# Kernel tuning notes

Measured on AMD Instinct MI355X. Metric: run time of the kernel, lower is better.

The kernel has to match this reference:

```python
import jax, jax.numpy as jnp
import numpy as np

B, CIN, COUT, S, K, G = 2, 64, 64, 128, 3, 4  # batch, in_ch, out_ch, shapes(H=W), kernel, groups


def _conv1x1(w, x, b=None):
    # nn.Conv2d(kernel_size=1): w [O,C], x [B,C,H,W]
    y = jnp.einsum('oc,bchw->bohw', w, x)
    return y if b is None else y + b[None, :, None, None]


def _forward(fs, ft, w_q, w_k, w_v, rel_h, rel_w, weights1_real, weights1_imag,
             w0_w, w0_b, convv_w, convv_b, convv1_w, convv1_b, rate1, rate2):
    Bq, C, H, W = fs.shape
    q = _conv1x1(w_q, fs)  # [B,C,H,W]
    # key/value convs are 1x1 with no bias, so conv(pad(x)) == pad(conv(x))
    kf = jnp.pad(_conv1x1(w_k, fs), ((0, 0), (0, 0), (1, 1), (1, 1)))
    vf = jnp.pad(_conv1x1(w_v, fs), ((0, 0), (0, 0), (1, 1), (1, 1)))

    def unfold(xp):  # [B,C,H+2,W+2] -> [B,C,H,W,K,K] (torch .unfold(2,K,1).unfold(3,K,1))
        p = jnp.stack([xp[:, :, i:i + H, j:j + W] for i in range(K) for j in range(K)], axis=-1)
        return p.reshape(Bq, C, H, W, K, K)

    k = unfold(kf)
    v = unfold(vf)
    # relative position bias on the two channel halves (broadcast as in torch)
    k = jnp.concatenate([k[:, :C // 2] + rel_h, k[:, C // 2:] + rel_w], axis=1)
    k = k.reshape(Bq, G, C // G, H, W, K * K)
    v = v.reshape(Bq, G, C // G, H, W, K * K)
    qg = q.reshape(Bq, G, C // G, H, W, 1)
    attn = jax.nn.softmax(qg * k, axis=-1)                         # [B,G,C/G,H,W,9]
    out = jnp.einsum('bnchwk,bnchwk->bnchw', attn, v).reshape(Bq, C, H, W)

    # ---- spectral branch ----
    # Original code: einsum 'bchw,ohwi->bochw' (i is summed over weights only),
    # flatten to [B, o*c*H, W], fftshift over dims(1,2), reshape to [B,64,8192,128,2],
    # zero an EMPTY slice (rw=int(0.1*1)=0), ifftshift over dims(3,2,1), then
    # ifft2 with s=(H,W) which CROPS the 8192 dim to its first H rows.
    # The roll arithmetic composes to: net-zero shift on o and w axes, and a
    # +C/2 shift on the c axis; the crop then selects c = C//2, h = 0..H-1.
    # => out1 = Re ifft2( fft2(out)[:, C//2] * sum_i W[o,:,h,w] ).
    fs_ft = jnp.fft.fft2(out, norm='ortho')                        # [B,C,H,W] complex
    wsum = (weights1_real + 1j * weights1_imag).sum(axis=1)        # [CIN,H,W] (sum over 'i')
    out_ft = fs_ft[:, C // 2][:, None, :, :] * wsum[None]          # [B,CIN,H,W]
    out1 = jnp.fft.ifft2(out_ft, norm='ortho').real                # [B,CIN,H,W]

    out_cv = _conv1x1(convv_w, out, convv_b)                       # con_vv
    out2 = _conv1x1(w0_w, out_cv, w0_b)                            # w0
    out2 = _conv1x1(convv1_w, out2, convv1_b)                      # con_vv1

    make_fs = rate1[0] * out1 + rate2[0] * out2                    # [B,CIN,H,W]
    make_fs = jnp.transpose(make_fs, (0, 2, 3, 1))                 # [B,H,W,C]
    ftv = ft.reshape(Bq, H, W, C)                                  # out_channels != 320 branch
    return jnp.mean((make_fs - ftv) ** 2)


def setup_inputs() -> dict:
    key = jax.random.key(0)
    ks = jax.random.split(key, 12)
    n = lambda i, shape, s=1.0: jax.random.normal(ks[i], shape, dtype=jnp.float32) * s
    scale = 1.0 / (CIN * COUT)
    return {
        'fs': n(0, (B, CIN, S, S)),
        'ft': n(1, (B, S, S, COUT)),
        'w_q': n(2, (COUT, CIN), 0.1),
        'w_k': n(3, (COUT, CIN), 0.1),
        'w_v': n(4, (COUT, CIN), 0.1),
        'rel_h': n(5, (COUT // 2, 1, 1, K, 1)),
        'rel_w': n(6, (COUT // 2, 1, 1, 1, K)),
        'weights1_real': jax.random.uniform(ks[7], (CIN, COUT, S, S), dtype=jnp.float32) * scale,
        'weights1_imag': jax.random.uniform(ks[8], (CIN, COUT, S, S), dtype=jnp.float32) * scale,
        'w0_w': n(9, (COUT, CIN), 0.1),
        'w0_b': jnp.zeros((COUT,), jnp.float32),
        'convv_w': n(10, (CIN, COUT), 0.1),
        'convv_b': jnp.zeros((CIN,), jnp.float32),
        'convv1_w': n(11, (CIN, COUT), 0.1),
        'convv1_b': jnp.zeros((CIN,), jnp.float32),
        'rate1': jnp.full((1,), 0.5, jnp.float32),
        'rate2': jnp.full((1,), 0.5, jnp.float32),
    }


def reference(fs, ft, w_q, w_k, w_v, rel_h, rel_w, weights1_real, weights1_imag,
              w0_w, w0_b, convv_w, convv_b, convv1_w, convv1_b, rate1, rate2):
    return _forward(fs, ft, w_q, w_k, w_v, rel_h, rel_w, weights1_real, weights1_imag,
                    w0_w, w0_b, convv_w, convv_b, convv1_w, convv1_b, rate1, rate2)
```

## Files before the change

### kernel.cpp

```cpp
#include <hip/hip_runtime.h>
#include <math.h>

constexpr int HW   = 128 * 128;
constexpr int NCHW = 2 * 64 * HW;

constexpr size_t OFF_Q    = 0;
constexpr size_t OFF_K    = 2097152;
constexpr size_t OFF_V    = 4194304;
constexpr size_t OFF_FTT  = 4194304;
constexpr size_t OFF_OUT  = 6291456;
constexpr size_t OFF_OUT2 = 8388608;
constexpr size_t OFF_R    = 8388608;
constexpr size_t OFF_F    = 10485760;
constexpr size_t OFF_M    = 10551296;
constexpr size_t OFF_BC   = 10555392;
constexpr size_t OFF_Z    = 0;

__global__ __launch_bounds__(256) void k_gemm64(
    const float* __restrict__ x, const float* __restrict__ w,
    const float* __restrict__ bias, float* __restrict__ y)
{
    __shared__ float xs[64][64];
    __shared__ float wl[64][65];
    int blk = blockIdx.x;
    int b = blk >> 8;
    int px0 = (blk & 255) << 6;
    int t = threadIdx.x;
    for (int i = t; i < 4096; i += 256) {
        int r = i >> 6, cix = i & 63;
        wl[r][cix] = w[i];
        xs[r][cix] = x[b * (64 * HW) + r * HW + px0 + cix];
    }
    __syncthreads();
    int pxq = t & 15, rq = t >> 4;
    float acc[4][4];
    #pragma unroll
    for (int i = 0; i < 4; i++)
        for (int j = 0; j < 4; j++) acc[i][j] = 0.f;
    for (int ci = 0; ci < 64; ci++) {
        float4 xv = *reinterpret_cast<const float4*>(&xs[ci][pxq * 4]);
        #pragma unroll
        for (int i = 0; i < 4; i++) {
            float wv = wl[rq * 4 + i][ci];
            acc[i][0] += wv * xv.x; acc[i][1] += wv * xv.y;
            acc[i][2] += wv * xv.z; acc[i][3] += wv * xv.w;
        }
    }
    #pragma unroll
    for (int i = 0; i < 4; i++) {
        int co = rq * 4 + i;
        float bb = bias ? bias[co] : 0.f;
        float* p = y + b * (64 * HW) + co * HW + px0 + pxq * 4;
        p[0] = acc[i][0] + bb; p[1] = acc[i][1] + bb;
        p[2] = acc[i][2] + bb; p[3] = acc[i][3] + bb;
    }
}

__global__ __launch_bounds__(256) void k_attn(
    const float* __restrict__ q, const float* __restrict__ kc, const float* __restrict__ vc,
    const float* __restrict__ rel_h, const float* __restrict__ rel_w,
    float* __restrict__ out)
{
    int idx = blockIdx.x * 256 + threadIdx.x;
    if (idx >= NCHW) return;
    int w = idx & 127;
    int h = (idx >> 7) & 127;
    int c = (idx >> 14) & 63;
    float qv = q[idx];
    float s[9], vv[9];
    #pragma unroll
    for (int ki = 0; ki < 3; ki++) {
        #pragma unroll
        for (int kj = 0; kj < 3; kj++) {
            int hh = h + ki - 1, ww = w + kj - 1;
            bool inb = (hh >= 0 && hh < 128 && ww >= 0 && ww < 128);
            int nidx = (idx & ~(HW - 1)) + hh * 128 + ww;
            float kvv = inb ? kc[nidx] : 0.f;
            float vvv = inb ? vc[nidx] : 0.f;
            float rel = (c < 32) ? rel_h[c * 3 + ki] : rel_w[(c - 32) * 3 + kj];
            s[ki * 3 + kj] = qv * (kvv + rel);
            vv[ki * 3 + kj] = vvv;
        }
    }
    float m = s[0];
    #pragma unroll
    for (int i = 1; i < 9; i++) m = fmaxf(m, s[i]);
    float den = 0.f, num = 0.f;
    #pragma unroll
    for (int i = 0; i < 9; i++) { float e = __expf(s[i] - m); den += e; num += e * vv[i]; }
    out[idx] = num / den;
}

__global__ __launch_bounds__(256) void k_tft(const float* __restrict__ ft, float* __restrict__ ftT)
{
    __shared__ float tile[64][65];
    int blk = blockIdx.x; int b = blk >> 8; int p0 = (blk & 255) << 6;
    int t = threadIdx.x;
    for (int e = t; e < 4096; e += 256) {
        int pp = e >> 6, cc = e & 63;
        tile[pp][cc] = ft[(b * HW + p0 + pp) * 64 + cc];
    }
    __syncthreads();
    for (int e = t; e < 4096; e += 256) {
        int cc = e >> 6, pp = e & 63;
        ftT[b * (64 * HW) + cc * HW + p0 + pp] = tile[pp][cc];
    }
}

__global__ __launch_bounds__(128) void k_fftrow_fwd(const float* __restrict__ out, float* __restrict__ R)
{
    int bh = blockIdx.x; int b = bh >> 7, h = bh & 127;
    int k = threadIdx.x;
    __shared__ float xr[128];
    xr[k] = out[((b * 64 + 32) << 14) + h * 128 + k];
    __syncthreads();
    float s0, c0; __sincosf(-6.2831853071795864769f * (float)k / 128.0f, &s0, &c0);
    float twr = 1.f, twi = 0.f, ar = 0.f, ai = 0.f;
    for (int n = 0; n < 128; n++) {
        float xv = xr[n];
        ar += xv * twr; ai += xv * twi;
        float nr = twr * c0 - twi * s0;
        twi = twr * s0 + twi * c0; twr = nr;
    }
    float2* Rp = (float2*)R;
    Rp[(b << 14) + h * 128 + k] = make_float2(ar, ai);
}

__global__ __launch_bounds__(128) void k_fftcol_fwd(const float* __restrict__ R, float* __restrict__ F)
{
    int bk = blockIdx.x; int b = bk >> 7, k2 = bk & 127;
    int k1 = threadIdx.x;
    __shared__ float2 col[128];
    const float2* Rp = (const float2*)R;
    col[k1] = Rp[(b << 14) + k1 * 128 + k2];
    __syncthreads();
    float s0, c0; __sincosf(-6.2831853071795864769f * (float)k1 / 128.0f, &s0, &c0);
    float twr = 1.f, twi = 0.f, ar = 0.f, ai = 0.f;
    for (int n = 0; n < 128; n++) {
        float2 xv = col[n];
        ar += xv.x * twr - xv.y * twi;
        ai += xv.x * twi + xv.y * twr;
        float nr = twr * c0 - twi * s0;
        twi = twr * s0 + twi * c0; twr = nr;
    }
    float2* Fp = (float2*)F;
    Fp[(b << 14) + k1 * 128 + k2] = make_float2(ar * (1.f / 128.f), ai * (1.f / 128.f));
}

__global__ __launch_bounds__(256) void k_combine(
    const float* __restrict__ convv_w, const float* __restrict__ convv_b,
    const float* __restrict__ w0_w, const float* __restrict__ w0_b,
    const float* __restrict__ convv1_w, const float* __restrict__ convv1_b,
    float* __restrict__ M, float* __restrict__ bc)
{
    __shared__ float T[64][65];
    __shared__ float t2[64];
    int t = threadIdx.x;
    for (int e = t; e < 4096; e += 256) {
        int i = e >> 6, j = e & 63;
        float a = 0.f;
        for (int kk = 0; kk < 64; kk++) a += w0_w[i * 64 + kk] * convv_w[kk * 64 + j];
        T[i][j] = a;
    }
    if (t < 64) {
        float a = 0.f;
        for (int kk = 0; kk < 64; kk++) a += w0_w[t * 64 + kk] * convv_b[kk];
        t2[t] = a + w0_b[t];
    }
    __syncthreads();
    for (int e = t; e < 4096; e += 256) {
        int i = e >> 6, j = e & 63;
        float a = 0.f;
        for (int kk = 0; kk < 64; kk++) a += convv1_w[i * 64 + kk] * T[kk][j];
        M[e] = a;
    }
    if (t < 64) {
        float a = 0.f;
        for (int kk = 0; kk < 64; kk++) a += convv1_w[t * 64 + kk] * t2[kk];
        bc[t] = a + convv1_b[t];
    }
}

__global__ __launch_bounds__(128) void k_wsum_ifftrow(
    const float* __restrict__ w1r, const float* __restrict__ w1i,
    const float* __restrict__ F, float* __restrict__ Z)
{
    int blk = blockIdx.x; int c = blk >> 7, h = blk & 127;
    int t = threadIdx.x;
    float sr = 0.f, si = 0.f;
    int base = (c << 20) + h * 128 + t;
    #pragma unroll 8
    for (int o = 0; o < 64; o++) {
        sr += w1r[base + (o << 14)];
        si += w1i[base + (o << 14)];
    }
    __shared__ float4 g[128];
    const float2* Fp = (const float2*)F;
    float2 f0 = Fp[h * 128 + t];
    float2 f1 = Fp[(1 << 14) + h * 128 + t];
    g[t] = make_float4(f0.x * sr - f0.y * si, f0.x * si + f0.y * sr,
                       f1.x * sr - f1.y * si, f1.x * si + f1.y * sr);
    __syncthreads();
    float s0, c0; __sincosf(6.2831853071795864769f * (float)t / 128.0f, &s0, &c0);
    float twr = 1.f, twi = 0.f;
    float a0r = 0.f, a0i = 0.f, a1r = 0.f, a1i = 0.f;
    for (int n = 0; n < 128; n++) {
        float4 gv = g[n];
        a0r += gv.x * twr - gv.y * twi;
        a0i += gv.x * twi + gv.y * twr;
        a1r += gv.z * twr - gv.w * twi;
        a1i += gv.z * twi + gv.w * twr;
        float nr = twr * c0 - twi * s0;
        twi = twr * s0 + twi * c0; twr = nr;
    }
    float2* Zp = (float2*)Z;
    Zp[(c << 14) + h * 128 + t]               = make_float2(a0r, a0i);
    Zp[((64 + c) << 14) + h * 128 + t]        = make_float2(a1r, a1i);
}

__global__ __launch_bounds__(256) void k_ifftcol_mse(
    const float* __restrict__ Zb, const float* __restrict__ out2,
    const float* __restrict__ ftT, const float* __restrict__ rate1,
    const float* __restrict__ rate2, float* __restrict__ result)
{
    int blk = blockIdx.x;
    int xc = blk & 3;
    int c  = (blk >> 2) & 63;
    int b  = blk >> 8;
    int t = threadIdx.x;
    int xl = t & 31;
    int yq = t >> 5;
    __shared__ float2 zs[128][33];
    const float2* Zp = (const float2*)Zb;
    int zbase = ((b * 64 + c) << 14) + xc * 32;
    for (int e = t; e < 4096; e += 256) {
        int hh = e >> 5, xx = e & 31;
        zs[hh][xx] = Zp[zbase + hh * 128 + xx];
    }
    __syncthreads();

    float twx[4], twy[4], stx[4], sty[4];
    float Sr[4][4], Si[4][4];
    #pragma unroll
    for (int j = 0; j < 4; j++) {
        int y0 = yq + 8 * j;
        float ss, cc;
        __sincosf(6.2831853071795864769f * (float)y0 / 128.0f, &ss, &cc);
        stx[j] = cc; sty[j] = ss;
        twx[j] = 1.f; twy[j] = 0.f;
        #pragma unroll
        for (int m = 0; m < 4; m++) { Sr[j][m] = 0.f; Si[j][m] = 0.f; }
    }
    for (int h = 0; h < 128; h += 4) {
        #pragma unroll
        for (int m = 0; m < 4; m++) {
            float2 z = zs[h + m][xl];
            #pragma unroll
            for (int j = 0; j < 4; j++) {
                Sr[j][m] += z.x * twx[j] - z.y * twy[j];
                Si[j][m] += z.x * twy[j] + z.y * twx[j];
                float nr = twx[j] * stx[j] - twy[j] * sty[j];
                twy[j]   = twx[j] * sty[j] + twy[j] * stx[j];
                twx[j]   = nr;
            }
        }
    }
    float r1 = rate1[0], r2 = rate2[0];
    int x = xc * 32 + xl;
    int obase = ((b * 64 + c) << 14) + x;
    float part = 0.f;
    #pragma unroll
    for (int j = 0; j < 4; j++) {
        int y0 = yq + 8 * j;
        float o[4];
        o[0] = Sr[j][0] + Sr[j][1] + Sr[j][2] + Sr[j][3];
        o[1] = Sr[j][0] - Si[j][1] - Sr[j][2] + Si[j][3];
        o[2] = Sr[j][0] - Sr[j][1] + Sr[j][2] - Sr[j][3];
        o[3] = Sr[j][0] + Si[j][1] - Sr[j][2] - Si[j][3];
        #pragma unroll
        for (int m = 0; m < 4; m++) {
            int y = y0 + 32 * m;
            float out1 = o[m] * (1.f / 128.f);
            int gi = obase + y * 128;
            float mk = r1 * out1 + r2 * out2[gi];
            float d = mk - ftT[gi];
            part += d * d;
        }
    }
    __shared__ float red[256];
    red[t] = part;
    __syncthreads();
    for (int s = 128; s > 0; s >>= 1) {
        if (t < s) red[t] += red[t + s];
        __syncthreads();
    }
    if (t == 0) atomicAdd(result, red[0] * (1.f / 2097152.f));
}

extern "C" void kernel_launch(void* const* d_in, const int* in_sizes, int n_in,
                              void* d_out, int out_size, void* d_ws, size_t ws_size,
                              hipStream_t stream) {
    const float* fs       = (const float*)d_in[0];
    const float* ft       = (const float*)d_in[1];
    const float* w_q      = (const float*)d_in[2];
    const float* w_k      = (const float*)d_in[3];
    const float* w_v      = (const float*)d_in[4];
    const float* rel_h    = (const float*)d_in[5];
    const float* rel_w    = (const float*)d_in[6];
    const float* w1r      = (const float*)d_in[7];
    const float* w1i      = (const float*)d_in[8];
    const float* w0_w     = (const float*)d_in[9];
    const float* w0_b     = (const float*)d_in[10];
    const float* convv_w  = (const float*)d_in[11];
    const float* convv_b  = (const float*)d_in[12];
    const float* convv1_w = (const float*)d_in[13];
    const float* convv1_b = (const float*)d_in[14];
    const float* rate1    = (const float*)d_in[15];
    const float* rate2    = (const float*)d_in[16];

    float* ws = (float*)d_ws;
    float* q    = ws + OFF_Q;
    float* kk   = ws + OFF_K;
    float* vv   = ws + OFF_V;
    float* ftT  = ws + OFF_FTT;
    float* out  = ws + OFF_OUT;
    float* out2 = ws + OFF_OUT2;
    float* R    = ws + OFF_R;
    float* F    = ws + OFF_F;
    float* M    = ws + OFF_M;
    float* bc   = ws + OFF_BC;
    float* Z    = ws + OFF_Z;

    k_gemm64<<<512, 256, 0, stream>>>(fs, w_q, nullptr, q);
    k_gemm64<<<512, 256, 0, stream>>>(fs, w_k, nullptr, kk);
    k_gemm64<<<512, 256, 0, stream>>>(fs, w_v, nullptr, vv);
    k_attn<<<8192, 256, 0, stream>>>(q, kk, vv, rel_h, rel_w, out);
    k_tft<<<512, 256, 0, stream>>>(ft, ftT);
    k_fftrow_fwd<<<256, 128, 0, stream>>>(out, R);
    k_fftcol_fwd<<<256, 128, 0, stream>>>(R, F);
    k_combine<<<1, 256, 0, stream>>>(convv_w, convv_b, w0_w, w0_b, convv1_w, convv1_b, M, bc);
    k_gemm64<<<512, 256, 0, stream>>>(out, M, bc, out2);
    k_wsum_ifftrow<<<8192, 128, 0, stream>>>(w1r, w1i, F, Z);
    hipMemsetAsync(d_out, 0, sizeof(float), stream);
    k_ifftcol_mse<<<512, 256, 0, stream>>>(Z, out2, ftT, rate1, rate2, (float*)d_out);
}
```

Baseline: 717.1 us.

## Fuse QKV projections, drop ft transpose, vectorize weight-sum reduction, stage combine weights

Merges the three separate 1x1 projection GEMMs into one kernel that loads the input tile once and writes q, k and v together. It also removes the ft transpose kernel and reads ft directly with a channel-strided index in the final MSE kernel. The dominant weight-sum kernel now reads w1r/w1i with float4 loads spread over four output groups and reduces them in shared memory. The tiny combine kernel now stages its weight matrices in shared memory. The strided ft reads may be less coalesced, and the weight-sum kernel uses more shared memory and an extra barrier.

```diff
diff --git a/kernel.cpp b/kernel.cpp
--- a/kernel.cpp
+++ b/kernel.cpp
@@ -7,7 +7,6 @@
 constexpr size_t OFF_Q    = 0;
 constexpr size_t OFF_K    = 2097152;
 constexpr size_t OFF_V    = 4194304;
-constexpr size_t OFF_FTT  = 4194304;
 constexpr size_t OFF_OUT  = 6291456;
 constexpr size_t OFF_OUT2 = 8388608;
 constexpr size_t OFF_R    = 8388608;
@@ -15,6 +14,52 @@
 constexpr size_t OFF_M    = 10551296;
 constexpr size_t OFF_BC   = 10555392;
 constexpr size_t OFF_Z    = 0;
+
+__global__ __launch_bounds__(256) void k_qkv(
+    const float* __restrict__ fs,
+    const float* __restrict__ w_q, const float* __restrict__ w_k, const float* __restrict__ w_v,
+    float* __restrict__ q, float* __restrict__ kk, float* __restrict__ vv)
+{
+    __shared__ float xs[64][64];
+    __shared__ float wl[3][64][65];
+    int blk = blockIdx.x;
+    int b = blk >> 8;
+    int px0 = (blk & 255) << 6;
+    int t = threadIdx.x;
+    for (int i = t; i < 4096; i += 256) {
+        int r = i >> 6, cix = i & 63;
+        wl[0][r][cix] = w_q[i];
+        wl[1][r][cix] = w_k[i];
+        wl[2][r][cix] = w_v[i];
+        xs[r][cix] = fs[b * (64 * HW) + r * HW + px0 + cix];
+    }
+    __syncthreads();
+    int pxq = t & 15, rq = t >> 4;
+    float aq[4][4], ak[4][4], av[4][4];
+    #pragma unroll
+    for (int i = 0; i < 4; i++)
+        for (int j = 0; j < 4; j++) { aq[i][j] = 0.f; ak[i][j] = 0.f; av[i][j] = 0.f; }
+    for (int ci = 0; ci < 64; ci++) {
+        float4 xv = *reinterpret_cast<const float4*>(&xs[ci][pxq * 4]);
+        #pragma unroll
+        for (int i = 0; i < 4; i++) {
+            float wq_ = wl[0][rq * 4 + i][ci];
+            float wk_ = wl[1][rq * 4 + i][ci];
+            float wv_ = wl[2][rq * 4 + i][ci];
+            aq[i][0] += wq_ * xv.x; aq[i][1] += wq_ * xv.y; aq[i][2] += wq_ * xv.z; aq[i][3] += wq_ * xv.w;
+            ak[i][0] += wk_ * xv.x; ak[i][1] += wk_ * xv.y; ak[i][2] += wk_ * xv.z; ak[i][3] += wk_ * xv.w;
+            av[i][0] += wv_ * xv.x; av[i][1] += wv_ * xv.y; av[i][2] += wv_ * xv.z; av[i][3] += wv_ * xv.w;
+        }
+    }
+    #pragma unroll
+    for (int i = 0; i < 4; i++) {
+        int co = rq * 4 + i;
+        size_t base = (size_t)b * (64 * HW) + (size_t)co * HW + px0 + pxq * 4;
+        *reinterpret_cast<float4*>(q  + base) = make_float4(aq[i][0], aq[i][1], aq[i][2], aq[i][3]);
+        *reinterpret_cast<float4*>(kk + base) = make_float4(ak[i][0], ak[i][1], ak[i][2], ak[i][3]);
+        *reinterpret_cast<float4*>(vv + base) = make_float4(av[i][0], av[i][1], av[i][2], av[i][3]);
+    }
+}
 
 __global__ __launch_bounds__(256) void k_gemm64(
     const float* __restrict__ x, const float* __restrict__ w,
@@ -91,22 +136,6 @@
     out[idx] = num / den;
 }
 
-__global__ __launch_bounds__(256) void k_tft(const float* __restrict__ ft, float* __restrict__ ftT)
-{
-    __shared__ float tile[64][65];
-    int blk = blockIdx.x; int b = blk >> 8; int p0 = (blk & 255) << 6;
-    int t = threadIdx.x;
-    for (int e = t; e < 4096; e += 256) {
-        int pp = e >> 6, cc = e & 63;
-        tile[pp][cc] = ft[(b * HW + p0 + pp) * 64 + cc];
-    }
-    __syncthreads();
-    for (int e = t; e < 4096; e += 256) {
-        int cc = e >> 6, pp = e & 63;
-        ftT[b * (64 * HW) + cc * HW + p0 + pp] = tile[pp][cc];
-    }
-}
-
 __global__ __launch_bounds__(128) void k_fftrow_fwd(const float* __restrict__ out, float* __restrict__ R)
 {
     int bh = blockIdx.x; int b = bh >> 7, h = bh & 127;
@@ -153,30 +182,40 @@
     const float* __restrict__ convv1_w, const float* __restrict__ convv1_b,
     float* __restrict__ M, float* __restrict__ bc)
 {
+    __shared__ float A[64][64];
+    __shared__ float Bm[64][64];
+    __shared__ float Cm[64][64];
     __shared__ float T[64][65];
     __shared__ float t2[64];
     int t = threadIdx.x;
     for (int e = t; e < 4096; e += 256) {
         int i = e >> 6, j = e & 63;
-        float a = 0.f;
-        for (int kk = 0; kk < 64; kk++) a += w0_w[i * 64 + kk] * convv_w[kk * 64 + j];
-        T[i][j] = a;
-    }
-    if (t < 64) {
-        float a = 0.f;
-        for (int kk = 0; kk < 64; kk++) a += w0_w[t * 64 + kk] * convv_b[kk];
-        t2[t] = a + w0_b[t];
+        A[i][j]  = convv_w[e];
+        Bm[i][j] = w0_w[e];
+        Cm[i][j] = convv1_w[e];
     }
     __syncthreads();
     for (int e = t; e < 4096; e += 256) {
         int i = e >> 6, j = e & 63;
         float a = 0.f;
-        for (int kk = 0; kk < 64; kk++) a += convv1_w[i * 64 + kk] * T[kk][j];
-        M[e] = a;
+        for (int kk = 0; kk < 64; kk++) a += Bm[i][kk] * A[kk][j];
+        T[i][j] = a;
     }
     if (t < 64) {
         float a = 0.f;
-        for (int kk = 0; kk < 64; kk++) a += convv1_w[t * 64 + kk] * t2[kk];
+        for (int kk = 0; kk < 64; kk++) a += Bm[t][kk] * convv_b[kk];
+        t2[t] = a + w0_b[t];
+    }
+    __syncthreads();
+    for (int e = t; e < 4096; e += 256) {
+        int i = e >> 6, j = e & 63;
+        float a = 0.f;
+        for (int kk = 0; kk < 64; kk++) a += Cm[i][kk] * T[kk][j];
+        M[e] = a;
+    }
+    if (t < 64) {
+        float a = 0.f;
+        for (int kk = 0; kk < 64; kk++) a += Cm[t][kk] * t2[kk];
         bc[t] = a + convv1_b[t];
     }
 }
@@ -187,40 +226,70 @@
 {
     int blk = blockIdx.x; int c = blk >> 7, h = blk & 127;
     int t = threadIdx.x;
-    float sr = 0.f, si = 0.f;
-    int base = (c << 20) + h * 128 + t;
+    int wq = t & 31, og = t >> 5;
+    const float4* r4 = (const float4*)(w1r + ((size_t)c << 20) + (h << 7));
+    const float4* i4 = (const float4*)(w1i + ((size_t)c << 20) + (h << 7));
+    float4 sr = make_float4(0.f, 0.f, 0.f, 0.f);
+    float4 si = make_float4(0.f, 0.f, 0.f, 0.f);
+    int base = ((og * 16) << 12) + wq;
     #pragma unroll 8
-    for (int o = 0; o < 64; o++) {
-        sr += w1r[base + (o << 14)];
-        si += w1i[base + (o << 14)];
-    }
-    __shared__ float4 g[128];
-    const float2* Fp = (const float2*)F;
-    float2 f0 = Fp[h * 128 + t];
-    float2 f1 = Fp[(1 << 14) + h * 128 + t];
-    g[t] = make_float4(f0.x * sr - f0.y * si, f0.x * si + f0.y * sr,
-                       f1.x * sr - f1.y * si, f1.x * si + f1.y * sr);
+    for (int oo = 0; oo < 16; oo++) {
+        float4 a = r4[base + (oo << 12)];
+        float4 bb = i4[base + (oo << 12)];
+        sr.x += a.x;  sr.y += a.y;  sr.z += a.z;  sr.w += a.w;
+        si.x += bb.x; si.y += bb.y; si.z += bb.z; si.w += bb.w;
+    }
+    __shared__ float4 redr[4][32];
+    __shared__ float4 redi[4][32];
+    __shared__ float2 g0[128];
+    __shared__ float2 g1[128];
+    redr[og][wq] = sr; redi[og][wq] = si;
+    __syncthreads();
+    if (t < 32) {
+        float4 r0 = redr[0][t], r1_ = redr[1][t], r2_ = redr[2][t], r3 = redr[3][t];
+        float4 i0 = redi[0][t], i1 = redi[1][t], i2 = redi[2][t], i3 = redi[3][t];
+        float sumr[4], sumi[4];
+        sumr[0] = r0.x + r1_.x + r2_.x + r3.x;
+        sumr[1] = r0.y + r1_.y + r2_.y + r3.y;
+        sumr[2] = r0.z + r1_.z + r2_.z + r3.z;
+        sumr[3] = r0.w + r1_.w + r2_.w + r3.w;
+        sumi[0] = i0.x + i1.x + i2.x + i3.x;
+        sumi[1] = i0.y + i1.y + i2.y + i3.y;
+        sumi[2] = i0.z + i1.z + i2.z + i3.z;
+        sumi[3] = i0.w + i1.w + i2.w + i3.w;
+        const float2* Fp = (const float2*)F;
+        #pragma unroll
+        for (int j = 0; j < 4; j++) {
+            int w = t * 4 + j;
+            float wr = sumr[j], wi = sumi[j];
+            float2 f0 = Fp[(h << 7) + w];
+            float2 f1 = Fp[(1 << 14) + (h << 7) + w];
+            g0[w] = make_float2(f0.x * wr - f0.y * wi, f0.x * wi + f0.y * wr);
+            g1[w] = make_float2(f1.x * wr - f1.y * wi, f1.x * wi + f1.y * wr);
+        }
+    }
     __syncthreads();
     float s0, c0; __sincosf(6.2831853071795864769f * (float)t / 128.0f, &s0, &c0);
     float twr = 1.f, twi = 0.f;
     float a0r = 0.f, a0i = 0.f, a1r = 0.f, a1i = 0.f;
     for (int n = 0; n < 128; n++) {
-        float4 gv = g[n];
-        a0r += gv.x * twr - gv.y * twi;
-        a0i += gv.x * twi + gv.y * twr;
-        a1r += gv.z * twr - gv.w * twi;
-        a1i += gv.z * twi + gv.w * twr;
+        float2 u0 = g0[n];
+        float2 u1 = g1[n];
+        a0r += u0.x * twr - u0.y * twi;
+        a0i += u0.x * twi + u0.y * twr;
+        a1r += u1.x * twr - u1.y * twi;
+        a1i += u1.x * twi + u1.y * twr;
         float nr = twr * c0 - twi * s0;
         twi = twr * s0 + twi * c0; twr = nr;
     }
     float2* Zp = (float2*)Z;
-    Zp[(c << 14) + h * 128 + t]               = make_float2(a0r, a0i);
-    Zp[((64 + c) << 14) + h * 128 + t]        = make_float2(a1r, a1i);
+    Zp[(c << 14) + h * 128 + t]        = make_float2(a0r, a0i);
+    Zp[((64 + c) << 14) + h * 128 + t] = make_float2(a1r, a1i);
 }
 
 __global__ __launch_bounds__(256) void k_ifftcol_mse(
     const float* __restrict__ Zb, const float* __restrict__ out2,
-    const float* __restrict__ ftT, const float* __restrict__ rate1,
+    const float* __restrict__ ft, const float* __restrict__ rate1,
     const float* __restrict__ rate2, float* __restrict__ result)
 {
     int blk = blockIdx.x;
@@ -283,7 +352,8 @@
             float out1 = o[m] * (1.f / 128.f);
             int gi = obase + y * 128;
             float mk = r1 * out1 + r2 * out2[gi];
-            float d = mk - ftT[gi];
+            int fidx = ((b * HW + y * 128 + x) << 6) + c;
+            float d = mk - ft[fidx];
             part += d * d;
         }
     }
@@ -322,7 +392,6 @@
     float* q    = ws + OFF_Q;
     float* kk   = ws + OFF_K;
     float* vv   = ws + OFF_V;
-    float* ftT  = ws + OFF_FTT;
     float* out  = ws + OFF_OUT;
     float* out2 = ws + OFF_OUT2;
     float* R    = ws + OFF_R;
@@ -331,16 +400,13 @@
     float* bc   = ws + OFF_BC;
     float* Z    = ws + OFF_Z;
 
-    k_gemm64<<<512, 256, 0, stream>>>(fs, w_q, nullptr, q);
-    k_gemm64<<<512, 256, 0, stream>>>(fs, w_k, nullptr, kk);
-    k_gemm64<<<512, 256, 0, stream>>>(fs, w_v, nullptr, vv);
+    k_qkv<<<512, 256, 0, stream>>>(fs, w_q, w_k, w_v, q, kk, vv);
     k_attn<<<8192, 256, 0, stream>>>(q, kk, vv, rel_h, rel_w, out);
-    k_tft<<<512, 256, 0, stream>>>(ft, ftT);
     k_fftrow_fwd<<<256, 128, 0, stream>>>(out, R);
     k_fftcol_fwd<<<256, 128, 0, stream>>>(R, F);
     k_combine<<<1, 256, 0, stream>>>(convv_w, convv_b, w0_w, w0_b, convv1_w, convv1_b, M, bc);
     k_gemm64<<<512, 256, 0, stream>>>(out, M, bc, out2);
     k_wsum_ifftrow<<<8192, 128, 0, stream>>>(w1r, w1i, F, Z);
     hipMemsetAsync(d_out, 0, sizeof(float), stream);
-    k_ifftcol_mse<<<512, 256, 0, stream>>>(Z, out2, ftT, rate1, rate2, (float*)d_out);
-}
+    k_ifftcol_mse<<<512, 256, 0, stream>>>(Z, out2, ft, rate1, rate2, (float*)d_out);
+}
```

Result: faster. 674.0 us (-6.0%).
